# Performance work log

Hardware: AMD Instinct MI355X
Metric: run time of the kernel (lower is better)

## Reference

```python
import jax, jax.numpy as jnp
import numpy as np

D = 1024
K = 8
EPS_BN = 1e-5
EPS_L2 = 1e-8


def l2norm(x, axis=-1):
    return x / (jnp.sqrt(jnp.sum(x * x, axis=axis, keepdims=True)) + EPS_L2)


def setup_inputs() -> dict:
    key = jax.random.key(0)
    ks = jax.random.split(key, 12)
    B, T = 256, 72
    H = D // K
    s1 = 1.0 / np.sqrt(D)
    s2 = 1.0 / np.sqrt(H)
    return {
        "img_embed": jax.random.normal(ks[0], (B, 36, D), dtype=jnp.float32),
        "cap_embed": jax.random.normal(ks[1], (B, T, D), dtype=jnp.float32),
        "lens": jax.random.randint(ks[2], (B,), 1, T + 1),
        # fc_gamma: Linear(D,H) -> ReLU -> Linear(H,D); weights stored (in,out)
        "Wg1": jax.random.uniform(ks[3], (D, H), jnp.float32, -s1, s1),
        "bg1": jax.random.uniform(ks[4], (H,), jnp.float32, -s1, s1),
        "Wg2": jax.random.uniform(ks[5], (H, D), jnp.float32, -s2, s2),
        "bg2": jax.random.uniform(ks[6], (D,), jnp.float32, -s2, s2),
        # fc_beta
        "Wb1": jax.random.uniform(ks[7], (D, H), jnp.float32, -s1, s1),
        "bb1": jax.random.uniform(ks[8], (H,), jnp.float32, -s1, s1),
        "Wb2": jax.random.uniform(ks[9], (H, D), jnp.float32, -s2, s2),
        "bb2": jax.random.uniform(ks[10], (D,), jnp.float32, -s2, s2),
    }


def reference(img_embed, cap_embed, lens, Wg1, bg1, Wg2, bg2, Wb1, bb1, Wb2, bb2):
    # img_embed: (B, 36, D), cap_embed: (B, T, D), lens: (B,)
    B, T, _ = cap_embed.shape

    # img_repr: mean over 36 regions -> (B, D)
    img_repr = img_embed.mean(axis=1)

    # BatchNorm1d (affine=False, training): stats over (batch, time) per feature.
    # cap in torch is (B, D, T); stats reduce over batch+time axes.
    mean = cap_embed.mean(axis=(0, 1))                      # (D,)
    var = jnp.mean((cap_embed - mean) ** 2, axis=(0, 1))    # biased, (D,)
    norm_feat = (cap_embed - mean) / jnp.sqrt(var + EPS_BN)  # (B, T, D)

    # Masked mean pooling over valid timesteps (BN stats precede masking,
    # matching the original). Pooling is linear, so conditional affine
    # (gamma,beta constant over time) commutes with it.
    mask = (jnp.arange(T)[None, :] < lens[:, None]).astype(cap_embed.dtype)  # (B, T)
    pooled = jnp.einsum('btd,bt->bd', norm_feat, mask) / lens[:, None].astype(cap_embed.dtype)  # (B_cap, D)

    # Conditional gamma/beta per image
    gammas = jax.nn.relu(img_repr @ Wg1 + bg1) @ Wg2 + bg2   # (B_img, D)
    betas = jax.nn.relu(img_repr @ Wb1 + bb1) @ Wb2 + bb2    # (B_img, D)

    # txt[i, j, :] = pooled[j] * (gamma_i + 1) + beta_i
    txt = pooled[None, :, :] * (gammas[:, None, :] + 1.0) + betas[:, None, :]  # (B_img, B_cap, D)
    txt_n = l2norm(txt, axis=-1)
    img_n = l2norm(img_repr, axis=-1)                        # (B_img, D)

    # sim for image i over captions j; original writes sims[:, i] = sim
    sim_ij = jnp.einsum('id,ijd->ij', img_n, txt_n)          # (B_img, B_cap)
    return sim_ij.T                                          # sims[j, i]
```

## Files before the change

### kernel.cpp

```cpp
#include <hip/hip_runtime.h>
#include <math.h>

#define NDIM 1024
#define HDIM 128
#define NB 256
#define NT 72
#define NR 36
#define KS 16

__device__ __forceinline__ float wave_sum(float v) {
#pragma unroll
  for (int off = 32; off > 0; off >>= 1) v += __shfl_down(v, off, 64);
  return v;
}

__device__ __forceinline__ float dot4(const float4 a, const float4 b) {
  return a.x * b.x + a.y * b.y + a.z * b.z + a.w * b.w;
}

__global__ __launch_bounds__(256) void k_front(const float* __restrict__ img,
                                               const float* __restrict__ cap,
                                               const int* __restrict__ lens,
                                               float* __restrict__ fs, float* __restrict__ fq,
                                               float* __restrict__ ms, float* __restrict__ repr,
                                               float* __restrict__ imgn) {
  const int bid = blockIdx.x, tid = threadIdx.x;
  __shared__ float red[4];
  __shared__ float sInv;
  if (bid < 512) {
    const int b = bid & 255;
    const int half = bid >> 8;
    const int len = lens[b];
    const int t0 = half * 36;
    const float* base = cap + (size_t)b * NT * NDIM + (size_t)t0 * NDIM + tid * 4;
    float fsx = 0.f, fsy = 0.f, fsz = 0.f, fsw = 0.f;
    float fqx = 0.f, fqy = 0.f, fqz = 0.f, fqw = 0.f;
    float msx = 0.f, msy = 0.f, msz = 0.f, msw = 0.f;
#pragma unroll 12
    for (int tt = 0; tt < 36; ++tt) {
      const float4 v = *reinterpret_cast<const float4*>(base + tt * NDIM);
      fsx += v.x; fsy += v.y; fsz += v.z; fsw += v.w;
      fqx += v.x * v.x; fqy += v.y * v.y; fqz += v.z * v.z; fqw += v.w * v.w;
      if (t0 + tt < len) { msx += v.x; msy += v.y; msz += v.z; msw += v.w; }
    }
    const int o = (half * NB + b) * NDIM + tid * 4;
    *reinterpret_cast<float4*>(fs + o) = make_float4(fsx, fsy, fsz, fsw);
    *reinterpret_cast<float4*>(fq + o) = make_float4(fqx, fqy, fqz, fqw);
    *reinterpret_cast<float4*>(ms + o) = make_float4(msx, msy, msz, msw);
  } else {
    const int b = bid - 512;
    const float* base = img + (size_t)b * NR * NDIM + tid * 4;
    float sx = 0.f, sy = 0.f, sz = 0.f, sw = 0.f;
#pragma unroll 12
    for (int r = 0; r < NR; ++r) {
      const float4 v = *reinterpret_cast<const float4*>(base + r * NDIM);
      sx += v.x; sy += v.y; sz += v.z; sw += v.w;
    }
    const float inv = 1.0f / (float)NR;
    sx *= inv; sy *= inv; sz *= inv; sw *= inv;
    *reinterpret_cast<float4*>(repr + (size_t)b * NDIM + tid * 4) = make_float4(sx, sy, sz, sw);
    const float sq = wave_sum(sx * sx + sy * sy + sz * sz + sw * sw);
    const int lane = tid & 63, wv = tid >> 6;
    if (lane == 0) red[wv] = sq;
    __syncthreads();
    if (tid == 0) sInv = 1.0f / (sqrtf(red[0] + red[1] + red[2] + red[3]) + 1e-8f);
    __syncthreads();
    const float iv = sInv;
    *reinterpret_cast<float4*>(imgn + (size_t)b * NDIM + tid * 4) =
        make_float4(sx * iv, sy * iv, sz * iv, sw * iv);
  }
}

__global__ __launch_bounds__(512) void k_mid(const float* __restrict__ fs,
                                             const float* __restrict__ fq,
                                             const float* __restrict__ ms,
                                             const int* __restrict__ lens,
                                             const float* __restrict__ repr,
                                             const float* __restrict__ Wg1,
                                             const float* __restrict__ Wb1,
                                             float* __restrict__ pooled,
                                             float* __restrict__ hpart) {
  const int bid = blockIdx.x, tid = threadIdx.x;
  __shared__ float ss[8][64], sq2[8][64], smu[64], srs[64];
  __shared__ float shr[8][128];
  __shared__ float sacc[8][128][8];
  if (bid < 16) {
    const int d0 = bid * 64, dloc = tid & 63, grp = tid >> 6;
    float s = 0.f, q = 0.f;
    const int r0 = grp * 64;
#pragma unroll 8
    for (int r = r0; r < r0 + 64; ++r) {
      s += fs[(size_t)r * NDIM + d0 + dloc];
      q += fq[(size_t)r * NDIM + d0 + dloc];
    }
    ss[grp][dloc] = s;
    sq2[grp][dloc] = q;
    __syncthreads();
    if (tid < 64) {
      float S = 0.f, Q = 0.f;
#pragma unroll
      for (int g2 = 0; g2 < 8; ++g2) { S += ss[g2][tid]; Q += sq2[g2][tid]; }
      const float invN = 1.0f / (float)(NB * NT);
      const float mu = S * invN;
      const float var = Q * invN - mu * mu;
      smu[tid] = mu;
      srs[tid] = 1.0f / sqrtf(var + 1e-5f);
    }
    __syncthreads();
    const int dcol = tid & 63, brow = tid >> 6;
    const float mu = smu[dcol], rs = srs[dcol];
#pragma unroll 4
    for (int b = brow; b < NB; b += 8) {
      const float invl = 1.0f / (float)lens[b];
      const float m = ms[(size_t)b * NDIM + d0 + dcol] + ms[(size_t)(NB + b) * NDIM + d0 + dcol];
      pooled[(size_t)b * NDIM + d0 + dcol] = (m * invl - mu) * rs;
    }
  } else {
    const int idx = bid - 16;
    const int g = idx & 31, br = (idx >> 5) & 1, ks = idx >> 6;
    const int b0 = g * 8;
    const int kbase = ks * 128;
    const int h2 = tid & 63;
    const int ksub = tid >> 6;
    const float* __restrict__ W = br ? Wb1 : Wg1;
    {
      const int im = tid >> 6, c2 = (tid & 63) * 2;
      *reinterpret_cast<float2*>(&shr[im][c2]) =
          *reinterpret_cast<const float2*>(repr + (size_t)(b0 + im) * NDIM + kbase + c2);
    }
    __syncthreads();
    float acc0[8] = {0, 0, 0, 0, 0, 0, 0, 0}, acc1[8] = {0, 0, 0, 0, 0, 0, 0, 0};
#pragma unroll
    for (int q = 0; q < 4; ++q) {
      const int dl = ksub * 16 + q * 4;
      const float* wq = W + (size_t)(kbase + dl) * HDIM + h2;
      const float wa0 = wq[0], wa1 = wq[128], wa2 = wq[256], wa3 = wq[384];
      const float wb0 = wq[64], wb1 = wq[192], wb2 = wq[320], wb3 = wq[448];
#pragma unroll
      for (int i = 0; i < 8; ++i) {
        const float4 s = *reinterpret_cast<const float4*>(&shr[i][dl]);
        acc0[i] += s.x * wa0 + s.y * wa1 + s.z * wa2 + s.w * wa3;
        acc1[i] += s.x * wb0 + s.y * wb1 + s.z * wb2 + s.w * wb3;
      }
    }
#pragma unroll
    for (int i = 0; i < 8; ++i) {
      sacc[ksub][h2][i] = acc0[i];
      sacc[ksub][h2 + 64][i] = acc1[i];
    }
    __syncthreads();
#pragma unroll
    for (int v = tid; v < 1024; v += 512) {
      const int hh = v & 127, im = v >> 7;
      float s = 0.f;
#pragma unroll
      for (int k2 = 0; k2 < 8; ++k2) s += sacc[k2][hh][im];
      hpart[(((size_t)ks * 2 + br) * NB + b0 + im) * HDIM + hh] = s;
    }
  }
}

__global__ __launch_bounds__(512) void k_l2(
    const float* __restrict__ hpart, const float* __restrict__ bg1,
    const float* __restrict__ bb1, const float* __restrict__ Wg2,
    const float* __restrict__ bg2, const float* __restrict__ Wb2,
    const float* __restrict__ bb2, const float* __restrict__ imgn, float* __restrict__ uarr,
    float* __restrict__ aarr, float* __restrict__ bvarr, float* __restrict__ cpart,
    float* __restrict__ epart) {
  const int gb = blockIdx.x, dgrp = blockIdx.y;
  const int b0 = gb * 4;
  const int tid = threadIdx.x;
  const int dl = tid & 127;
  const int d = dgrp * 128 + dl;
  const int ig = tid >> 7;
  __shared__ float shh[2][4][HDIM];
  __shared__ float sred[8][2];
#pragma unroll
  for (int v = tid; v < 1024; v += 512) {
    const int brv = v >> 9, rem = v & 511, im = rem >> 7, hh = rem & 127;
    float s = 0.f;
#pragma unroll
    for (int k2 = 0; k2 < 8; ++k2)
      s += hpart[(((size_t)k2 * 2 + brv) * NB + b0 + im) * HDIM + hh];
    s += brv ? bb1[hh] : bg1[hh];
    shh[brv][im][hh] = fmaxf(s, 0.f);
  }
  __syncthreads();
  float ga = 0.f, ba = 0.f;
#pragma unroll 8
  for (int q = 0; q < 32; ++q) {
    const int h = q * 4;
    const float4 hg = *reinterpret_cast<const float4*>(&shh[0][ig][h]);
    const float4 hb = *reinterpret_cast<const float4*>(&shh[1][ig][h]);
    const float* wgp = Wg2 + (size_t)h * NDIM + d;
    const float* wbp = Wb2 + (size_t)h * NDIM + d;
    ga += hg.x * wgp[0] + hg.y * wgp[1024] + hg.z * wgp[2048] + hg.w * wgp[3072];
    ba += hb.x * wbp[0] + hb.y * wbp[1024] + hb.z * wbp[2048] + hb.w * wbp[3072];
  }
  const float ox = ga + bg2[d] + 1.0f;
  const float tb = ba + bb2[d];
  const size_t o = (size_t)(b0 + ig) * NDIM + d;
  const float nv = imgn[o];
  uarr[o] = nv * ox;
  aarr[o] = ox * ox;
  bvarr[o] = 2.0f * ox * tb;
  const float c = wave_sum(nv * tb);
  const float e = wave_sum(tb * tb);
  const int lane = tid & 63, wv = tid >> 6;
  if (lane == 0) { sred[wv][0] = c; sred[wv][1] = e; }
  __syncthreads();
  if (tid < 8) {
    const int im = tid >> 1, isE = tid & 1;
    const float vv = sred[im * 2][isE] + sred[im * 2 + 1][isE];
    (isE ? epart : cpart)[dgrp * NB + b0 + im] = vv;
  }
}

__global__ __launch_bounds__(256) void k_simtile(
    const float* __restrict__ uarr, const float* __restrict__ aarr,
    const float* __restrict__ bvarr, const float* __restrict__ pooled,
    float* __restrict__ pn, float* __restrict__ pd) {
  __shared__ float su[64][36], sa[64][36], sb[64][36], sp[64][36];
  const int tid = threadIdx.x;
  const int tx = tid & 15, ty = tid >> 4;
  const int i0 = blockIdx.x * 64, j0 = blockIdx.y * 64;
  const int k0 = blockIdx.z * (NDIM / KS);
  const int lr = tid >> 3;
  const int lc = (tid & 7) * 4;
  float an[4][4] = {{0}}, ad[4][4] = {{0}};
  for (int dc = k0; dc < k0 + NDIM / KS; dc += 32) {
    __syncthreads();
#pragma unroll
    for (int rep = 0; rep < 2; ++rep) {
      const int r = lr + rep * 32;
      *reinterpret_cast<float4*>(&su[r][lc]) =
          *reinterpret_cast<const float4*>(uarr + (size_t)(i0 + r) * NDIM + dc + lc);
      *reinterpret_cast<float4*>(&sa[r][lc]) =
          *reinterpret_cast<const float4*>(aarr + (size_t)(i0 + r) * NDIM + dc + lc);
      *reinterpret_cast<float4*>(&sb[r][lc]) =
          *reinterpret_cast<const float4*>(bvarr + (size_t)(i0 + r) * NDIM + dc + lc);
      *reinterpret_cast<float4*>(&sp[r][lc]) =
          *reinterpret_cast<const float4*>(pooled + (size_t)(j0 + r) * NDIM + dc + lc);
    }
    __syncthreads();
#pragma unroll
    for (int dd = 0; dd < 32; dd += 4) {
      float4 rp[4], rq[4];
#pragma unroll
      for (int n = 0; n < 4; ++n) {
        rp[n] = *reinterpret_cast<const float4*>(&sp[ty + 16 * n][dd]);
        rq[n] = make_float4(rp[n].x * rp[n].x, rp[n].y * rp[n].y, rp[n].z * rp[n].z,
                            rp[n].w * rp[n].w);
      }
#pragma unroll
      for (int m = 0; m < 4; ++m) {
        const float4 ru = *reinterpret_cast<const float4*>(&su[tx + 16 * m][dd]);
        const float4 ra = *reinterpret_cast<const float4*>(&sa[tx + 16 * m][dd]);
        const float4 rb = *reinterpret_cast<const float4*>(&sb[tx + 16 * m][dd]);
#pragma unroll
        for (int n = 0; n < 4; ++n) {
          an[m][n] += dot4(ru, rp[n]);
          ad[m][n] += dot4(ra, rq[n]) + dot4(rb, rp[n]);
        }
      }
    }
  }
  const int s = blockIdx.z;
#pragma unroll
  for (int m = 0; m < 4; ++m) {
#pragma unroll
    for (int n = 0; n < 4; ++n) {
      const int i = i0 + tx + 16 * m, j = j0 + ty + 16 * n;
      const size_t o = ((size_t)s * NB + j) * NB + i;
      pn[o] = an[m][n];
      pd[o] = ad[m][n];
    }
  }
}

__global__ __launch_bounds__(256) void k_reduce(const float* __restrict__ pn,
                                                const float* __restrict__ pd,
                                                const float* __restrict__ cpart,
                                                const float* __restrict__ epart,
                                                float* __restrict__ out) {
  const int j = blockIdx.x, i = threadIdx.x;
  const size_t base = (size_t)j * NB + i;
  float n = 0.f, den = 0.f;
#pragma unroll
  for (int s = 0; s < KS; ++s) {
    const size_t o = base + (size_t)s * (NB * NB);
    n += pn[o];
    den += pd[o];
  }
  float cv = 0.f, ev = 0.f;
#pragma unroll
  for (int s = 0; s < 8; ++s) { cv += cpart[s * NB + i]; ev += epart[s * NB + i]; }
  const float num = n + cv;
  const float den2 = den + ev;
  out[base] = num / (sqrtf(fmaxf(den2, 0.0f)) + 1e-8f);
}

extern "C" void kernel_launch(void* const* d_in, const int* in_sizes, int n_in,
                              void* d_out, int out_size, void* d_ws, size_t ws_size,
                              hipStream_t stream) {
  const float* img = (const float*)d_in[0];
  const float* cap = (const float*)d_in[1];
  const int* lens = (const int*)d_in[2];
  const float* Wg1 = (const float*)d_in[3];
  const float* bg1 = (const float*)d_in[4];
  const float* Wg2 = (const float*)d_in[5];
  const float* bg2 = (const float*)d_in[6];
  const float* Wb1 = (const float*)d_in[7];
  const float* bb1 = (const float*)d_in[8];
  const float* Wb2 = (const float*)d_in[9];
  const float* bb2 = (const float*)d_in[10];
  float* out = (float*)d_out;

  float* w = (float*)d_ws;
  float* fullsum = w; w += 2 * NB * NDIM;
  float* fullsq = w;  w += 2 * NB * NDIM;
  float* msum = w;    w += 2 * NB * NDIM;
  float* hpart = w;   w += 16 * NB * HDIM;
  float* pooled = w;  w += NB * NDIM;
  float* uarr = w;    w += NB * NDIM;
  float* aarr = w;    w += NB * NDIM;
  float* bvarr = w;   w += NB * NDIM;
  float* cpart = w;   w += 8 * NB;
  float* epart = w;   w += 8 * NB;
  float* repr = uarr;
  float* imgn = aarr;
  float* pn = fullsum;
  float* pd = msum;

  hipLaunchKernelGGL(k_front, dim3(768), dim3(256), 0, stream, img, cap, lens, fullsum, fullsq,
                     msum, repr, imgn);
  hipLaunchKernelGGL(k_mid, dim3(528), dim3(512), 0, stream, fullsum, fullsq, msum, lens, repr,
                     Wg1, Wb1, pooled, hpart);
  hipLaunchKernelGGL(k_l2, dim3(64, 8), dim3(512), 0, stream, hpart, bg1, bb1, Wg2, bg2, Wb2,
                     bb2, imgn, uarr, aarr, bvarr, cpart, epart);
  hipLaunchKernelGGL(k_simtile, dim3(4, 4, KS), dim3(256), 0, stream, uarr, aarr, bvarr, pooled,
                     pn, pd);
  hipLaunchKernelGGL(k_reduce, dim3(NB), dim3(256), 0, stream, pn, pd, cpart, epart, out);
}
```

Measured before the change: 86.39 us.

## Fuse five kernels into one persistent kernel with atomic grid barriers

Replaces the five-kernel pipeline with a single 256-block persistent kernel that separates the phases with software grid barriers built on an atomic counter and spin-wait. This removes four kernel launch gaps and drain/fill bubbles between them. In exchange, the work is remapped so each phase uses 256 blocks of 512 threads: the front reduction does cap and img in one block, the sim tile computes a full 64-wide k slice per block, and the counter needs a memset each call. The barrier relies on all 256 blocks being co-resident, and the reduced block count may lower memory parallelism in the bandwidth-heavy front phase.

```diff
diff --git a/kernel.cpp b/kernel.cpp
--- a/kernel.cpp
+++ b/kernel.cpp
@@ -6,7 +6,8 @@
 #define NB 256
 #define NT 72
 #define NR 36
-#define KS 16
+#define NBLK 256
+#define NTHR 512
 
 __device__ __forceinline__ float wave_sum(float v) {
 #pragma unroll
@@ -18,245 +19,314 @@
   return a.x * b.x + a.y * b.y + a.z * b.z + a.w * b.w;
 }
 
-__global__ __launch_bounds__(256) void k_front(const float* __restrict__ img,
-                                               const float* __restrict__ cap,
-                                               const int* __restrict__ lens,
-                                               float* __restrict__ fs, float* __restrict__ fq,
-                                               float* __restrict__ ms, float* __restrict__ repr,
-                                               float* __restrict__ imgn) {
+__device__ __forceinline__ void grid_barrier(unsigned int* cnt, unsigned int target) {
+  __syncthreads();
+  if (threadIdx.x == 0) {
+    __hip_atomic_fetch_add(cnt, 1u, __ATOMIC_RELEASE, __HIP_MEMORY_SCOPE_AGENT);
+    while (__hip_atomic_load(cnt, __ATOMIC_ACQUIRE, __HIP_MEMORY_SCOPE_AGENT) < target)
+      __builtin_amdgcn_s_sleep(8);
+  }
+  __syncthreads();
+}
+
+#define OFF_FS 0u
+#define OFF_FQ 524288u
+#define OFF_MS 1048576u
+#define OFF_REPR 1572864u
+#define OFF_IMGN 1835008u
+#define OFF_POOL 2097152u
+#define OFF_U 2359296u
+#define OFF_A 2621440u
+#define OFF_BV 2883584u
+#define OFF_HP 3145728u
+#define OFF_PN 3670016u
+#define OFF_PD 4718592u
+#define OFF_MEAN 5767168u
+#define OFF_RSTD 5768192u
+#define OFF_CP 5769216u
+#define OFF_EP 5771264u
+#define CNT_BYTE_OFF (5773312u * 4u)
+
+__global__ __launch_bounds__(NTHR) void k_mega(
+    const float* __restrict__ img, const float* __restrict__ cap, const int* __restrict__ lens,
+    const float* __restrict__ Wg1, const float* __restrict__ bg1, const float* __restrict__ Wg2,
+    const float* __restrict__ bg2, const float* __restrict__ Wb1, const float* __restrict__ bb1,
+    const float* __restrict__ Wb2, const float* __restrict__ bb2, float* ws,
+    float* __restrict__ out, unsigned int* cnt) {
+  __shared__ float smem[17408];
+  __shared__ float sredbuf[32];
+  __shared__ float sval;
+
   const int bid = blockIdx.x, tid = threadIdx.x;
-  __shared__ float red[4];
-  __shared__ float sInv;
-  if (bid < 512) {
-    const int b = bid & 255;
-    const int half = bid >> 8;
+  const int lane = tid & 63, wv = tid >> 6;
+
+  float* fs = ws + OFF_FS;
+  float* fq = ws + OFF_FQ;
+  float* ms = ws + OFF_MS;
+  float* repr = ws + OFF_REPR;
+  float* imgn = ws + OFF_IMGN;
+  float* pooled = ws + OFF_POOL;
+  float* uarr = ws + OFF_U;
+  float* aarr = ws + OFF_A;
+  float* bvarr = ws + OFF_BV;
+  float* hpart = ws + OFF_HP;
+  float* pn = ws + OFF_PN;
+  float* pd = ws + OFF_PD;
+  float* meanv = ws + OFF_MEAN;
+  float* rstdv = ws + OFF_RSTD;
+  float* cpart = ws + OFF_CP;
+  float* epart = ws + OFF_EP;
+
+  {
+    const int b = bid;
     const int len = lens[b];
-    const int t0 = half * 36;
-    const float* base = cap + (size_t)b * NT * NDIM + (size_t)t0 * NDIM + tid * 4;
+    const int th = tid >> 8;
+    const int c4 = (tid & 255) * 4;
+    const int t0 = th * 36;
+    const float* base = cap + (size_t)b * NT * NDIM + (size_t)t0 * NDIM + c4;
     float fsx = 0.f, fsy = 0.f, fsz = 0.f, fsw = 0.f;
     float fqx = 0.f, fqy = 0.f, fqz = 0.f, fqw = 0.f;
     float msx = 0.f, msy = 0.f, msz = 0.f, msw = 0.f;
-#pragma unroll 12
+#pragma unroll 6
     for (int tt = 0; tt < 36; ++tt) {
       const float4 v = *reinterpret_cast<const float4*>(base + tt * NDIM);
       fsx += v.x; fsy += v.y; fsz += v.z; fsw += v.w;
       fqx += v.x * v.x; fqy += v.y * v.y; fqz += v.z * v.z; fqw += v.w * v.w;
       if (t0 + tt < len) { msx += v.x; msy += v.y; msz += v.z; msw += v.w; }
     }
-    const int o = (half * NB + b) * NDIM + tid * 4;
+    const size_t o = (size_t)(th * NB + b) * NDIM + c4;
     *reinterpret_cast<float4*>(fs + o) = make_float4(fsx, fsy, fsz, fsw);
     *reinterpret_cast<float4*>(fq + o) = make_float4(fqx, fqy, fqz, fqw);
     *reinterpret_cast<float4*>(ms + o) = make_float4(msx, msy, msz, msw);
-  } else {
-    const int b = bid - 512;
-    const float* base = img + (size_t)b * NR * NDIM + tid * 4;
+
+    const int rh = tid >> 8;
+    const float* ibase = img + (size_t)b * NR * NDIM + (size_t)rh * 18 * NDIM + c4;
     float sx = 0.f, sy = 0.f, sz = 0.f, sw = 0.f;
-#pragma unroll 12
-    for (int r = 0; r < NR; ++r) {
-      const float4 v = *reinterpret_cast<const float4*>(base + r * NDIM);
+#pragma unroll 6
+    for (int r = 0; r < 18; ++r) {
+      const float4 v = *reinterpret_cast<const float4*>(ibase + r * NDIM);
       sx += v.x; sy += v.y; sz += v.z; sw += v.w;
     }
-    const float inv = 1.0f / (float)NR;
-    sx *= inv; sy *= inv; sz *= inv; sw *= inv;
-    *reinterpret_cast<float4*>(repr + (size_t)b * NDIM + tid * 4) = make_float4(sx, sy, sz, sw);
-    const float sq = wave_sum(sx * sx + sy * sy + sz * sz + sw * sw);
-    const int lane = tid & 63, wv = tid >> 6;
-    if (lane == 0) red[wv] = sq;
-    __syncthreads();
-    if (tid == 0) sInv = 1.0f / (sqrtf(red[0] + red[1] + red[2] + red[3]) + 1e-8f);
-    __syncthreads();
-    const float iv = sInv;
-    *reinterpret_cast<float4*>(imgn + (size_t)b * NDIM + tid * 4) =
-        make_float4(sx * iv, sy * iv, sz * iv, sw * iv);
-  }
-}
-
-__global__ __launch_bounds__(512) void k_mid(const float* __restrict__ fs,
-                                             const float* __restrict__ fq,
-                                             const float* __restrict__ ms,
-                                             const int* __restrict__ lens,
-                                             const float* __restrict__ repr,
-                                             const float* __restrict__ Wg1,
-                                             const float* __restrict__ Wb1,
-                                             float* __restrict__ pooled,
-                                             float* __restrict__ hpart) {
-  const int bid = blockIdx.x, tid = threadIdx.x;
-  __shared__ float ss[8][64], sq2[8][64], smu[64], srs[64];
-  __shared__ float shr[8][128];
-  __shared__ float sacc[8][128][8];
+    float4* simg = reinterpret_cast<float4*>(smem);
+    simg[rh * 256 + (tid & 255)] = make_float4(sx, sy, sz, sw);
+    __syncthreads();
+    float4 mv = make_float4(0.f, 0.f, 0.f, 0.f);
+    float nsq = 0.f;
+    if (tid < 256) {
+      const float4 a = simg[tid], b4 = simg[256 + tid];
+      const float inv = 1.0f / (float)NR;
+      mv = make_float4((a.x + b4.x) * inv, (a.y + b4.y) * inv, (a.z + b4.z) * inv,
+                       (a.w + b4.w) * inv);
+      *reinterpret_cast<float4*>(repr + (size_t)b * NDIM + tid * 4) = mv;
+      nsq = mv.x * mv.x + mv.y * mv.y + mv.z * mv.z + mv.w * mv.w;
+    }
+    const float sq = wave_sum(nsq);
+    if (lane == 0) sredbuf[wv] = sq;
+    __syncthreads();
+    if (tid == 0) sval = 1.0f / (sqrtf(sredbuf[0] + sredbuf[1] + sredbuf[2] + sredbuf[3]) + 1e-8f);
+    __syncthreads();
+    if (tid < 256) {
+      const float iv = sval;
+      *reinterpret_cast<float4*>(imgn + (size_t)b * NDIM + tid * 4) =
+          make_float4(mv.x * iv, mv.y * iv, mv.z * iv, mv.w * iv);
+    }
+  }
+  grid_barrier(cnt, 1 * NBLK);
+
   if (bid < 16) {
-    const int d0 = bid * 64, dloc = tid & 63, grp = tid >> 6;
+    const int d0 = bid * 64;
+    const int dloc = tid & 63, rg = tid >> 6;
     float s = 0.f, q = 0.f;
-    const int r0 = grp * 64;
+    const int r0 = rg * 64;
 #pragma unroll 8
     for (int r = r0; r < r0 + 64; ++r) {
       s += fs[(size_t)r * NDIM + d0 + dloc];
       q += fq[(size_t)r * NDIM + d0 + dloc];
     }
-    ss[grp][dloc] = s;
-    sq2[grp][dloc] = q;
+    float* sps = smem;
+    float* spq = smem + 512;
+    sps[rg * 64 + dloc] = s;
+    spq[rg * 64 + dloc] = q;
     __syncthreads();
     if (tid < 64) {
       float S = 0.f, Q = 0.f;
 #pragma unroll
-      for (int g2 = 0; g2 < 8; ++g2) { S += ss[g2][tid]; Q += sq2[g2][tid]; }
+      for (int g2 = 0; g2 < 8; ++g2) { S += sps[g2 * 64 + tid]; Q += spq[g2 * 64 + tid]; }
       const float invN = 1.0f / (float)(NB * NT);
       const float mu = S * invN;
       const float var = Q * invN - mu * mu;
-      smu[tid] = mu;
-      srs[tid] = 1.0f / sqrtf(var + 1e-5f);
-    }
-    __syncthreads();
-    const int dcol = tid & 63, brow = tid >> 6;
-    const float mu = smu[dcol], rs = srs[dcol];
-#pragma unroll 4
-    for (int b = brow; b < NB; b += 8) {
-      const float invl = 1.0f / (float)lens[b];
-      const float m = ms[(size_t)b * NDIM + d0 + dcol] + ms[(size_t)(NB + b) * NDIM + d0 + dcol];
-      pooled[(size_t)b * NDIM + d0 + dcol] = (m * invl - mu) * rs;
-    }
-  } else {
-    const int idx = bid - 16;
-    const int g = idx & 31, br = (idx >> 5) & 1, ks = idx >> 6;
-    const int b0 = g * 8;
-    const int kbase = ks * 128;
+      meanv[d0 + tid] = mu;
+      rstdv[d0 + tid] = 1.0f / sqrtf(var + 1e-5f);
+    }
+    __syncthreads();
+  }
+  {
+    const int g = bid >> 3, ks = bid & 7;
+    const int b0 = g * 8, kbase = ks * 128;
+    float* shr = smem;
+    float* sacc = smem + 1024;
+    {
+      const int im = tid >> 6, c2 = (tid & 63) * 2;
+      *reinterpret_cast<float2*>(shr + im * 128 + c2) =
+          *reinterpret_cast<const float2*>(repr + (size_t)(b0 + im) * NDIM + kbase + c2);
+    }
+    __syncthreads();
     const int h2 = tid & 63;
     const int ksub = tid >> 6;
-    const float* __restrict__ W = br ? Wb1 : Wg1;
+    for (int br = 0; br < 2; ++br) {
+      const float* W = br ? Wb1 : Wg1;
+      float acc0[8] = {0, 0, 0, 0, 0, 0, 0, 0}, acc1[8] = {0, 0, 0, 0, 0, 0, 0, 0};
+#pragma unroll
+      for (int q = 0; q < 4; ++q) {
+        const int dl = ksub * 16 + q * 4;
+        const float* wq = W + (size_t)(kbase + dl) * HDIM + h2;
+        const float wa0 = wq[0], wa1 = wq[128], wa2 = wq[256], wa3 = wq[384];
+        const float wb0 = wq[64], wb1v = wq[192], wb2v = wq[320], wb3v = wq[448];
+#pragma unroll
+        for (int i = 0; i < 8; ++i) {
+          const float4 sv = *reinterpret_cast<const float4*>(shr + i * 128 + dl);
+          acc0[i] += sv.x * wa0 + sv.y * wa1 + sv.z * wa2 + sv.w * wa3;
+          acc1[i] += sv.x * wb0 + sv.y * wb1v + sv.z * wb2v + sv.w * wb3v;
+        }
+      }
+#pragma unroll
+      for (int i = 0; i < 8; ++i) {
+        sacc[((size_t)ksub * 128 + h2) * 8 + i] = acc0[i];
+        sacc[((size_t)ksub * 128 + h2 + 64) * 8 + i] = acc1[i];
+      }
+      __syncthreads();
+#pragma unroll
+      for (int v = tid; v < 1024; v += NTHR) {
+        const int hh = v & 127, im = v >> 7;
+        float s = 0.f;
+#pragma unroll
+        for (int k2 = 0; k2 < 8; ++k2) s += sacc[((size_t)k2 * 128 + hh) * 8 + im];
+        hpart[(((size_t)ks * 2 + br) * NB + b0 + im) * HDIM + hh] = s;
+      }
+      __syncthreads();
+    }
+  }
+  grid_barrier(cnt, 2 * NBLK);
+
+  {
+    if (tid < 256) {
+      const float invl = 1.0f / (float)lens[bid];
+      const int d = tid * 4;
+      const float4 m0 = *reinterpret_cast<const float4*>(ms + (size_t)bid * NDIM + d);
+      const float4 m1 = *reinterpret_cast<const float4*>(ms + (size_t)(NB + bid) * NDIM + d);
+      const float4 mu = *reinterpret_cast<const float4*>(meanv + d);
+      const float4 rs = *reinterpret_cast<const float4*>(rstdv + d);
+      *reinterpret_cast<float4*>(pooled + (size_t)bid * NDIM + d) =
+          make_float4(((m0.x + m1.x) * invl - mu.x) * rs.x, ((m0.y + m1.y) * invl - mu.y) * rs.y,
+                      ((m0.z + m1.z) * invl - mu.z) * rs.z, ((m0.w + m1.w) * invl - mu.w) * rs.w);
+    }
+    const int gb = bid >> 3, dgrp = bid & 7;
+    const int b0 = gb * 8;
+    float* shh = smem;
+    for (int v = tid; v < 2048; v += NTHR) {
+      const int brv = v >> 10, rem = v & 1023, im = rem >> 7, hh = rem & 127;
+      float s = 0.f;
+#pragma unroll
+      for (int k2 = 0; k2 < 8; ++k2)
+        s += hpart[(((size_t)k2 * 2 + brv) * NB + b0 + im) * HDIM + hh];
+      s += brv ? bb1[hh] : bg1[hh];
+      shh[v] = fmaxf(s, 0.f);
+    }
+    __syncthreads();
+    const int dl = tid & 127, ig = tid >> 7;
+    const int d = dgrp * 128 + dl;
+    float ga0 = 0.f, ba0 = 0.f, ga1 = 0.f, ba1 = 0.f;
+#pragma unroll 4
+    for (int q = 0; q < 32; ++q) {
+      const int h = q * 4;
+      const float* wgp = Wg2 + (size_t)h * NDIM + d;
+      const float* wbp = Wb2 + (size_t)h * NDIM + d;
+      const float wg0 = wgp[0], wg1v = wgp[1024], wg2v = wgp[2048], wg3v = wgp[3072];
+      const float wb0 = wbp[0], wb1v = wbp[1024], wb2v = wbp[2048], wb3v = wbp[3072];
+      const float4 hgA = *reinterpret_cast<const float4*>(shh + (0 * 8 + ig) * 128 + h);
+      const float4 hbA = *reinterpret_cast<const float4*>(shh + (1 * 8 + ig) * 128 + h);
+      const float4 hgB = *reinterpret_cast<const float4*>(shh + (0 * 8 + ig + 4) * 128 + h);
+      const float4 hbB = *reinterpret_cast<const float4*>(shh + (1 * 8 + ig + 4) * 128 + h);
+      ga0 += hgA.x * wg0 + hgA.y * wg1v + hgA.z * wg2v + hgA.w * wg3v;
+      ba0 += hbA.x * wb0 + hbA.y * wb1v + hbA.z * wb2v + hbA.w * wb3v;
+      ga1 += hgB.x * wg0 + hgB.y * wg1v + hgB.z * wg2v + hgB.w * wg3v;
+      ba1 += hbB.x * wb0 + hbB.y * wb1v + hbB.z * wb2v + hbB.w * wb3v;
+    }
+    const float bg2v = bg2[d], bb2v = bb2[d];
+    float cA, eA, cB, eB;
     {
-      const int im = tid >> 6, c2 = (tid & 63) * 2;
-      *reinterpret_cast<float2*>(&shr[im][c2]) =
-          *reinterpret_cast<const float2*>(repr + (size_t)(b0 + im) * NDIM + kbase + c2);
-    }
-    __syncthreads();
-    float acc0[8] = {0, 0, 0, 0, 0, 0, 0, 0}, acc1[8] = {0, 0, 0, 0, 0, 0, 0, 0};
-#pragma unroll
-    for (int q = 0; q < 4; ++q) {
-      const int dl = ksub * 16 + q * 4;
-      const float* wq = W + (size_t)(kbase + dl) * HDIM + h2;
-      const float wa0 = wq[0], wa1 = wq[128], wa2 = wq[256], wa3 = wq[384];
-      const float wb0 = wq[64], wb1 = wq[192], wb2 = wq[320], wb3 = wq[448];
-#pragma unroll
-      for (int i = 0; i < 8; ++i) {
-        const float4 s = *reinterpret_cast<const float4*>(&shr[i][dl]);
-        acc0[i] += s.x * wa0 + s.y * wa1 + s.z * wa2 + s.w * wa3;
-        acc1[i] += s.x * wb0 + s.y * wb1 + s.z * wb2 + s.w * wb3;
-      }
-    }
-#pragma unroll
-    for (int i = 0; i < 8; ++i) {
-      sacc[ksub][h2][i] = acc0[i];
-      sacc[ksub][h2 + 64][i] = acc1[i];
-    }
-    __syncthreads();
-#pragma unroll
-    for (int v = tid; v < 1024; v += 512) {
-      const int hh = v & 127, im = v >> 7;
-      float s = 0.f;
-#pragma unroll
-      for (int k2 = 0; k2 < 8; ++k2) s += sacc[k2][hh][im];
-      hpart[(((size_t)ks * 2 + br) * NB + b0 + im) * HDIM + hh] = s;
-    }
-  }
-}
-
-__global__ __launch_bounds__(512) void k_l2(
-    const float* __restrict__ hpart, const float* __restrict__ bg1,
-    const float* __restrict__ bb1, const float* __restrict__ Wg2,
-    const float* __restrict__ bg2, const float* __restrict__ Wb2,
-    const float* __restrict__ bb2, const float* __restrict__ imgn, float* __restrict__ uarr,
-    float* __restrict__ aarr, float* __restrict__ bvarr, float* __restrict__ cpart,
-    float* __restrict__ epart) {
-  const int gb = blockIdx.x, dgrp = blockIdx.y;
-  const int b0 = gb * 4;
-  const int tid = threadIdx.x;
-  const int dl = tid & 127;
-  const int d = dgrp * 128 + dl;
-  const int ig = tid >> 7;
-  __shared__ float shh[2][4][HDIM];
-  __shared__ float sred[8][2];
-#pragma unroll
-  for (int v = tid; v < 1024; v += 512) {
-    const int brv = v >> 9, rem = v & 511, im = rem >> 7, hh = rem & 127;
-    float s = 0.f;
-#pragma unroll
-    for (int k2 = 0; k2 < 8; ++k2)
-      s += hpart[(((size_t)k2 * 2 + brv) * NB + b0 + im) * HDIM + hh];
-    s += brv ? bb1[hh] : bg1[hh];
-    shh[brv][im][hh] = fmaxf(s, 0.f);
-  }
-  __syncthreads();
-  float ga = 0.f, ba = 0.f;
-#pragma unroll 8
-  for (int q = 0; q < 32; ++q) {
-    const int h = q * 4;
-    const float4 hg = *reinterpret_cast<const float4*>(&shh[0][ig][h]);
-    const float4 hb = *reinterpret_cast<const float4*>(&shh[1][ig][h]);
-    const float* wgp = Wg2 + (size_t)h * NDIM + d;
-    const float* wbp = Wb2 + (size_t)h * NDIM + d;
-    ga += hg.x * wgp[0] + hg.y * wgp[1024] + hg.z * wgp[2048] + hg.w * wgp[3072];
-    ba += hb.x * wbp[0] + hb.y * wbp[1024] + hb.z * wbp[2048] + hb.w * wbp[3072];
-  }
-  const float ox = ga + bg2[d] + 1.0f;
-  const float tb = ba + bb2[d];
-  const size_t o = (size_t)(b0 + ig) * NDIM + d;
-  const float nv = imgn[o];
-  uarr[o] = nv * ox;
-  aarr[o] = ox * ox;
-  bvarr[o] = 2.0f * ox * tb;
-  const float c = wave_sum(nv * tb);
-  const float e = wave_sum(tb * tb);
-  const int lane = tid & 63, wv = tid >> 6;
-  if (lane == 0) { sred[wv][0] = c; sred[wv][1] = e; }
-  __syncthreads();
-  if (tid < 8) {
-    const int im = tid >> 1, isE = tid & 1;
-    const float vv = sred[im * 2][isE] + sred[im * 2 + 1][isE];
-    (isE ? epart : cpart)[dgrp * NB + b0 + im] = vv;
-  }
-}
-
-__global__ __launch_bounds__(256) void k_simtile(
-    const float* __restrict__ uarr, const float* __restrict__ aarr,
-    const float* __restrict__ bvarr, const float* __restrict__ pooled,
-    float* __restrict__ pn, float* __restrict__ pd) {
-  __shared__ float su[64][36], sa[64][36], sb[64][36], sp[64][36];
-  const int tid = threadIdx.x;
-  const int tx = tid & 15, ty = tid >> 4;
-  const int i0 = blockIdx.x * 64, j0 = blockIdx.y * 64;
-  const int k0 = blockIdx.z * (NDIM / KS);
-  const int lr = tid >> 3;
-  const int lc = (tid & 7) * 4;
-  float an[4][4] = {{0}}, ad[4][4] = {{0}};
-  for (int dc = k0; dc < k0 + NDIM / KS; dc += 32) {
-    __syncthreads();
+      const float ox = ga0 + bg2v + 1.0f, tb = ba0 + bb2v;
+      const size_t o = (size_t)(b0 + ig) * NDIM + d;
+      const float nv = imgn[o];
+      uarr[o] = nv * ox;
+      aarr[o] = ox * ox;
+      bvarr[o] = 2.0f * ox * tb;
+      cA = nv * tb;
+      eA = tb * tb;
+    }
+    {
+      const float ox = ga1 + bg2v + 1.0f, tb = ba1 + bb2v;
+      const size_t o = (size_t)(b0 + ig + 4) * NDIM + d;
+      const float nv = imgn[o];
+      uarr[o] = nv * ox;
+      aarr[o] = ox * ox;
+      bvarr[o] = 2.0f * ox * tb;
+      cB = nv * tb;
+      eB = tb * tb;
+    }
+    cA = wave_sum(cA); eA = wave_sum(eA);
+    cB = wave_sum(cB); eB = wave_sum(eB);
+    if (lane == 0) {
+      sredbuf[wv * 4 + 0] = cA; sredbuf[wv * 4 + 1] = eA;
+      sredbuf[wv * 4 + 2] = cB; sredbuf[wv * 4 + 3] = eB;
+    }
+    __syncthreads();
+    if (tid < 16) {
+      const int im = tid >> 1, isE = tid & 1;
+      const int ig2 = im & 3, off = (im >> 2) * 2 + isE;
+      const float v = sredbuf[(ig2 * 2) * 4 + off] + sredbuf[(ig2 * 2 + 1) * 4 + off];
+      (isE ? epart : cpart)[dgrp * NB + b0 + im] = v;
+    }
+  }
+  grid_barrier(cnt, 3 * NBLK);
+
+  {
+    const int i0 = (bid & 3) * 64, j0 = ((bid >> 2) & 3) * 64, s = bid >> 4;
+    const int k0 = s * 64;
+    float* su = smem;
+    float* sa = smem + 4352;
+    float* sb = smem + 8704;
+    float* sp = smem + 13056;
+    const int lr = tid >> 3, lc4 = (tid & 7) * 4;
 #pragma unroll
     for (int rep = 0; rep < 2; ++rep) {
-      const int r = lr + rep * 32;
-      *reinterpret_cast<float4*>(&su[r][lc]) =
-          *reinterpret_cast<const float4*>(uarr + (size_t)(i0 + r) * NDIM + dc + lc);
-      *reinterpret_cast<float4*>(&sa[r][lc]) =
-          *reinterpret_cast<const float4*>(aarr + (size_t)(i0 + r) * NDIM + dc + lc);
-      *reinterpret_cast<float4*>(&sb[r][lc]) =
-          *reinterpret_cast<const float4*>(bvarr + (size_t)(i0 + r) * NDIM + dc + lc);
-      *reinterpret_cast<float4*>(&sp[r][lc]) =
-          *reinterpret_cast<const float4*>(pooled + (size_t)(j0 + r) * NDIM + dc + lc);
-    }
-    __syncthreads();
-#pragma unroll
-    for (int dd = 0; dd < 32; dd += 4) {
+      const int c = lc4 + rep * 32;
+      *reinterpret_cast<float4*>(su + lr * 68 + c) =
+          *reinterpret_cast<const float4*>(uarr + (size_t)(i0 + lr) * NDIM + k0 + c);
+      *reinterpret_cast<float4*>(sa + lr * 68 + c) =
+          *reinterpret_cast<const float4*>(aarr + (size_t)(i0 + lr) * NDIM + k0 + c);
+      *reinterpret_cast<float4*>(sb + lr * 68 + c) =
+          *reinterpret_cast<const float4*>(bvarr + (size_t)(i0 + lr) * NDIM + k0 + c);
+      *reinterpret_cast<float4*>(sp + lr * 68 + c) =
+          *reinterpret_cast<const float4*>(pooled + (size_t)(j0 + lr) * NDIM + k0 + c);
+    }
+    __syncthreads();
+    const int tx = tid & 31, ty = tid >> 5;
+    float an[2][4] = {{0.f}}, ad[2][4] = {{0.f}};
+#pragma unroll
+    for (int dd = 0; dd < 64; dd += 4) {
       float4 rp[4], rq[4];
 #pragma unroll
       for (int n = 0; n < 4; ++n) {
-        rp[n] = *reinterpret_cast<const float4*>(&sp[ty + 16 * n][dd]);
+        rp[n] = *reinterpret_cast<const float4*>(sp + (ty + 16 * n) * 68 + dd);
         rq[n] = make_float4(rp[n].x * rp[n].x, rp[n].y * rp[n].y, rp[n].z * rp[n].z,
                             rp[n].w * rp[n].w);
       }
 #pragma unroll
-      for (int m = 0; m < 4; ++m) {
-        const float4 ru = *reinterpret_cast<const float4*>(&su[tx + 16 * m][dd]);
-        const float4 ra = *reinterpret_cast<const float4*>(&sa[tx + 16 * m][dd]);
-        const float4 rb = *reinterpret_cast<const float4*>(&sb[tx + 16 * m][dd]);
+      for (int m = 0; m < 2; ++m) {
+        const float4 ru = *reinterpret_cast<const float4*>(su + (tx + 32 * m) * 68 + dd);
+        const float4 ra = *reinterpret_cast<const float4*>(sa + (tx + 32 * m) * 68 + dd);
+        const float4 rb = *reinterpret_cast<const float4*>(sb + (tx + 32 * m) * 68 + dd);
 #pragma unroll
         for (int n = 0; n < 4; ++n) {
           an[m][n] += dot4(ru, rp[n]);
@@ -264,40 +334,33 @@
         }
       }
     }
-  }
-  const int s = blockIdx.z;
-#pragma unroll
-  for (int m = 0; m < 4; ++m) {
-#pragma unroll
-    for (int n = 0; n < 4; ++n) {
-      const int i = i0 + tx + 16 * m, j = j0 + ty + 16 * n;
-      const size_t o = ((size_t)s * NB + j) * NB + i;
-      pn[o] = an[m][n];
-      pd[o] = ad[m][n];
-    }
-  }
-}
-
-__global__ __launch_bounds__(256) void k_reduce(const float* __restrict__ pn,
-                                                const float* __restrict__ pd,
-                                                const float* __restrict__ cpart,
-                                                const float* __restrict__ epart,
-                                                float* __restrict__ out) {
-  const int j = blockIdx.x, i = threadIdx.x;
-  const size_t base = (size_t)j * NB + i;
-  float n = 0.f, den = 0.f;
-#pragma unroll
-  for (int s = 0; s < KS; ++s) {
-    const size_t o = base + (size_t)s * (NB * NB);
-    n += pn[o];
-    den += pd[o];
-  }
-  float cv = 0.f, ev = 0.f;
-#pragma unroll
-  for (int s = 0; s < 8; ++s) { cv += cpart[s * NB + i]; ev += epart[s * NB + i]; }
-  const float num = n + cv;
-  const float den2 = den + ev;
-  out[base] = num / (sqrtf(fmaxf(den2, 0.0f)) + 1e-8f);
+#pragma unroll
+    for (int m = 0; m < 2; ++m) {
+#pragma unroll
+      for (int n = 0; n < 4; ++n) {
+        const int i = i0 + tx + 32 * m, j = j0 + ty + 16 * n;
+        const size_t o = ((size_t)s * NB + j) * NB + i;
+        pn[o] = an[m][n];
+        pd[o] = ad[m][n];
+      }
+    }
+  }
+  grid_barrier(cnt, 4 * NBLK);
+
+  if (tid < 256) {
+    const int j = bid, i = tid;
+    const size_t base = (size_t)j * NB + i;
+    float n = 0.f, dsum = 0.f;
+#pragma unroll
+    for (int s = 0; s < 16; ++s) {
+      n += pn[base + (size_t)s * (NB * NB)];
+      dsum += pd[base + (size_t)s * (NB * NB)];
+    }
+    float cv = 0.f, ev = 0.f;
+#pragma unroll
+    for (int s8 = 0; s8 < 8; ++s8) { cv += cpart[s8 * NB + i]; ev += epart[s8 * NB + i]; }
+    out[base] = (n + cv) / (sqrtf(fmaxf(dsum + ev, 0.0f)) + 1e-8f);
+  }
 }
 
 extern "C" void kernel_launch(void* const* d_in, const int* in_sizes, int n_in,
@@ -315,30 +378,10 @@
   const float* Wb2 = (const float*)d_in[9];
   const float* bb2 = (const float*)d_in[10];
   float* out = (float*)d_out;
-
-  float* w = (float*)d_ws;
-  float* fullsum = w; w += 2 * NB * NDIM;
-  float* fullsq = w;  w += 2 * NB * NDIM;
-  float* msum = w;    w += 2 * NB * NDIM;
-  float* hpart = w;   w += 16 * NB * HDIM;
-  float* pooled = w;  w += NB * NDIM;
-  float* uarr = w;    w += NB * NDIM;
-  float* aarr = w;    w += NB * NDIM;
-  float* bvarr = w;   w += NB * NDIM;
-  float* cpart = w;   w += 8 * NB;
-  float* epart = w;   w += 8 * NB;
-  float* repr = uarr;
-  float* imgn = aarr;
-  float* pn = fullsum;
-  float* pd = msum;
-
-  hipLaunchKernelGGL(k_front, dim3(768), dim3(256), 0, stream, img, cap, lens, fullsum, fullsq,
-                     msum, repr, imgn);
-  hipLaunchKernelGGL(k_mid, dim3(528), dim3(512), 0, stream, fullsum, fullsq, msum, lens, repr,
-                     Wg1, Wb1, pooled, hpart);
-  hipLaunchKernelGGL(k_l2, dim3(64, 8), dim3(512), 0, stream, hpart, bg1, bb1, Wg2, bg2, Wb2,
-                     bb2, imgn, uarr, aarr, bvarr, cpart, epart);
-  hipLaunchKernelGGL(k_simtile, dim3(4, 4, KS), dim3(256), 0, stream, uarr, aarr, bvarr, pooled,
-                     pn, pd);
-  hipLaunchKernelGGL(k_reduce, dim3(NB), dim3(256), 0, stream, pn, pd, cpart, epart, out);
-}
+  float* ws = (float*)d_ws;
+  unsigned int* cnt = (unsigned int*)((char*)d_ws + CNT_BYTE_OFF);
+
+  hipMemsetAsync(cnt, 0, 256, stream);
+  hipLaunchKernelGGL(k_mega, dim3(NBLK), dim3(NTHR), 0, stream, img, cap, lens, Wg1, bg1, Wg2,
+                     bg2, Wb1, bb1, Wb2, bb2, ws, out, cnt);
+}
```

Result: slower. 134.2 us (+55.4%).

## Restructure second MLP layer kernel for 8 images per block with float4 weight loads

Applied to the files above, without the earlier changes.

The k_l2 kernel now handles 8 images per block instead of 4, halving the grid and doubling reuse of each Wg2/Wb2 weight row loaded from global memory. Each thread computes 4 consecutive output features with float4 weight loads and splits the hidden dimension across two halves, combined through shared memory. Stores and the c/e reductions become float4 and 32-lane shuffles. This aims to cut weight traffic and load instruction count, in exchange for fewer blocks (256) and more shared memory per block.

```diff
diff --git a/kernel.cpp b/kernel.cpp
--- a/kernel.cpp
+++ b/kernel.cpp
@@ -168,51 +168,75 @@
     float* __restrict__ aarr, float* __restrict__ bvarr, float* __restrict__ cpart,
     float* __restrict__ epart) {
   const int gb = blockIdx.x, dgrp = blockIdx.y;
-  const int b0 = gb * 4;
+  const int b0 = gb * 8;
   const int tid = threadIdx.x;
-  const int dl = tid & 127;
-  const int d = dgrp * 128 + dl;
-  const int ig = tid >> 7;
-  __shared__ float shh[2][4][HDIM];
-  __shared__ float sred[8][2];
-#pragma unroll
-  for (int v = tid; v < 1024; v += 512) {
-    const int brv = v >> 9, rem = v & 511, im = rem >> 7, hh = rem & 127;
-    float s = 0.f;
-#pragma unroll
-    for (int k2 = 0; k2 < 8; ++k2)
-      s += hpart[(((size_t)k2 * 2 + brv) * NB + b0 + im) * HDIM + hh];
-    s += brv ? bb1[hh] : bg1[hh];
-    shh[brv][im][hh] = fmaxf(s, 0.f);
+  __shared__ float shh[2][8][HDIM];
+  __shared__ float sga[8][HDIM];
+  __shared__ float sba[8][HDIM];
+
+  {
+    const int hh4 = (tid & 31) * 4;
+    const int imA = (tid >> 5) & 7;
+    const int brA = tid >> 8;
+    float4 acc = make_float4(0.f, 0.f, 0.f, 0.f);
+    const float* hp = hpart + ((size_t)brA * NB + b0 + imA) * HDIM + hh4;
+#pragma unroll
+    for (int ks = 0; ks < 8; ++ks) {
+      const float4 v = *reinterpret_cast<const float4*>(hp + (size_t)ks * 2 * NB * HDIM);
+      acc.x += v.x; acc.y += v.y; acc.z += v.z; acc.w += v.w;
+    }
+    const float4 bias = *reinterpret_cast<const float4*>((brA ? bb1 : bg1) + hh4);
+    *reinterpret_cast<float4*>(&shh[brA][imA][hh4]) =
+        make_float4(fmaxf(acc.x + bias.x, 0.f), fmaxf(acc.y + bias.y, 0.f),
+                    fmaxf(acc.z + bias.z, 0.f), fmaxf(acc.w + bias.w, 0.f));
   }
   __syncthreads();
-  float ga = 0.f, ba = 0.f;
+
+  const int dq = tid & 31;
+  const int im = (tid >> 5) & 7;
+  const int hs = tid >> 8;
+  const int d = dgrp * 128 + dq * 4;
+  float4 ga = make_float4(0.f, 0.f, 0.f, 0.f), ba = make_float4(0.f, 0.f, 0.f, 0.f);
+  const int h0 = hs * 64;
 #pragma unroll 8
-  for (int q = 0; q < 32; ++q) {
-    const int h = q * 4;
-    const float4 hg = *reinterpret_cast<const float4*>(&shh[0][ig][h]);
-    const float4 hb = *reinterpret_cast<const float4*>(&shh[1][ig][h]);
-    const float* wgp = Wg2 + (size_t)h * NDIM + d;
-    const float* wbp = Wb2 + (size_t)h * NDIM + d;
-    ga += hg.x * wgp[0] + hg.y * wgp[1024] + hg.z * wgp[2048] + hg.w * wgp[3072];
-    ba += hb.x * wbp[0] + hb.y * wbp[1024] + hb.z * wbp[2048] + hb.w * wbp[3072];
-  }
-  const float ox = ga + bg2[d] + 1.0f;
-  const float tb = ba + bb2[d];
-  const size_t o = (size_t)(b0 + ig) * NDIM + d;
-  const float nv = imgn[o];
-  uarr[o] = nv * ox;
-  aarr[o] = ox * ox;
-  bvarr[o] = 2.0f * ox * tb;
-  const float c = wave_sum(nv * tb);
-  const float e = wave_sum(tb * tb);
-  const int lane = tid & 63, wv = tid >> 6;
-  if (lane == 0) { sred[wv][0] = c; sred[wv][1] = e; }
+  for (int h = h0; h < h0 + 64; ++h) {
+    const float4 wg = *reinterpret_cast<const float4*>(Wg2 + (size_t)h * NDIM + d);
+    const float4 wb = *reinterpret_cast<const float4*>(Wb2 + (size_t)h * NDIM + d);
+    const float hg = shh[0][im][h], hb = shh[1][im][h];
+    ga.x += hg * wg.x; ga.y += hg * wg.y; ga.z += hg * wg.z; ga.w += hg * wg.w;
+    ba.x += hb * wb.x; ba.y += hb * wb.y; ba.z += hb * wb.z; ba.w += hb * wb.w;
+  }
+  if (hs) {
+    *reinterpret_cast<float4*>(&sga[im][dq * 4]) = ga;
+    *reinterpret_cast<float4*>(&sba[im][dq * 4]) = ba;
+  }
   __syncthreads();
-  if (tid < 8) {
-    const int im = tid >> 1, isE = tid & 1;
-    const float vv = sred[im * 2][isE] + sred[im * 2 + 1][isE];
-    (isE ? epart : cpart)[dgrp * NB + b0 + im] = vv;
+  if (!hs) {
+    const float4 g2 = *reinterpret_cast<const float4*>(&sga[im][dq * 4]);
+    const float4 b2 = *reinterpret_cast<const float4*>(&sba[im][dq * 4]);
+    const float4 bgv = *reinterpret_cast<const float4*>(bg2 + d);
+    const float4 bbv = *reinterpret_cast<const float4*>(bb2 + d);
+    const float ox = ga.x + g2.x + bgv.x + 1.0f, oy = ga.y + g2.y + bgv.y + 1.0f;
+    const float oz = ga.z + g2.z + bgv.z + 1.0f, ow = ga.w + g2.w + bgv.w + 1.0f;
+    const float tx = ba.x + b2.x + bbv.x, ty = ba.y + b2.y + bbv.y;
+    const float tz = ba.z + b2.z + bbv.z, tw = ba.w + b2.w + bbv.w;
+    const size_t o = (size_t)(b0 + im) * NDIM + d;
+    const float4 nv = *reinterpret_cast<const float4*>(imgn + o);
+    *reinterpret_cast<float4*>(uarr + o) = make_float4(nv.x * ox, nv.y * oy, nv.z * oz, nv.w * ow);
+    *reinterpret_cast<float4*>(aarr + o) = make_float4(ox * ox, oy * oy, oz * oz, ow * ow);
+    *reinterpret_cast<float4*>(bvarr + o) =
+        make_float4(2.0f * ox * tx, 2.0f * oy * ty, 2.0f * oz * tz, 2.0f * ow * tw);
+    float c = nv.x * tx + nv.y * ty + nv.z * tz + nv.w * tw;
+    float e = tx * tx + ty * ty + tz * tz + tw * tw;
+#pragma unroll
+    for (int off = 16; off > 0; off >>= 1) {
+      c += __shfl_down(c, off, 32);
+      e += __shfl_down(e, off, 32);
+    }
+    if ((tid & 31) == 0) {
+      cpart[dgrp * NB + b0 + im] = c;
+      epart[dgrp * NB + b0 + im] = e;
+    }
   }
 }
 
@@ -336,7 +360,7 @@
                      msum, repr, imgn);
   hipLaunchKernelGGL(k_mid, dim3(528), dim3(512), 0, stream, fullsum, fullsq, msum, lens, repr,
                      Wg1, Wb1, pooled, hpart);
-  hipLaunchKernelGGL(k_l2, dim3(64, 8), dim3(512), 0, stream, hpart, bg1, bb1, Wg2, bg2, Wb2,
+  hipLaunchKernelGGL(k_l2, dim3(32, 8), dim3(512), 0, stream, hpart, bg1, bb1, Wg2, bg2, Wb2,
                      bb2, imgn, uarr, aarr, bvarr, cpart, epart);
   hipLaunchKernelGGL(k_simtile, dim3(4, 4, KS), dim3(256), 0, stream, uarr, aarr, bvarr, pooled,
                      pn, pd);
```

Measured after the change: 76.07 us. 11.9% less time.
